# Performance work log

Hardware: AMD Instinct MI355X
Metric: run time of the kernel (lower is better)

The kernel has to match this reference:

```python
import jax, jax.numpy as jnp
import numpy as np

HID = 150

def _lstm_layer(x, Wih, Whh, bih, bhh):
    # x: [T, D] -> [T, HID]; PyTorch gate order i, f, g, o
    b = bih + bhh
    xg = x @ Wih.T + b  # precompute input contribution: [T, 4H]
    def step(carry, xg_t):
        h, c = carry
        g = xg_t + h @ Whh.T
        i, f, gg, o = jnp.split(g, 4)
        i = jax.nn.sigmoid(i); f = jax.nn.sigmoid(f)
        gg = jnp.tanh(gg); o = jax.nn.sigmoid(o)
        c = f * c + i * gg
        h = o * jnp.tanh(c)
        return (h, c), h
    init = (jnp.zeros((HID,), x.dtype), jnp.zeros((HID,), x.dtype))
    _, ys = jax.lax.scan(step, init, xg)
    return ys

def _bilstm(x, Wih, Whh, bih, bhh):
    # x: [T, D]; params stacked [L, 2, ...]
    out = x
    for l in range(Wih.shape[0]):
        fwd = _lstm_layer(out, Wih[l, 0], Whh[l, 0], bih[l, 0], bhh[l, 0])
        bwd = _lstm_layer(out[::-1], Wih[l, 1], Whh[l, 1], bih[l, 1], bhh[l, 1])[::-1]
        out = jnp.concatenate([fwd, bwd], axis=-1)  # [T, 2H]
    return out

def setup_inputs() -> dict:
    key = jax.random.key(0)
    ks = jax.random.split(key, 16)
    s = 0.1  # keep LSTM gates in a sane range
    return {
        "inputs_solv": jax.random.normal(ks[0], (1, 4096, 300), jnp.float32),
        "inputs_solu": jax.random.normal(ks[1], (1, 4096, 300), jnp.float32),
        "solv_Wih": jax.random.normal(ks[2], (2, 2, 600, 300), jnp.float32) * s,
        "solv_Whh": jax.random.normal(ks[3], (2, 2, 600, 150), jnp.float32) * s,
        "solv_bih": jax.random.normal(ks[4], (2, 2, 600), jnp.float32) * s,
        "solv_bhh": jax.random.normal(ks[5], (2, 2, 600), jnp.float32) * s,
        "solu_Wih": jax.random.normal(ks[6], (2, 2, 600, 300), jnp.float32) * s,
        "solu_Whh": jax.random.normal(ks[7], (2, 2, 600, 150), jnp.float32) * s,
        "solu_bih": jax.random.normal(ks[8], (2, 2, 600), jnp.float32) * s,
        "solu_bhh": jax.random.normal(ks[9], (2, 2, 600), jnp.float32) * s,
        "fc1_w": jax.random.normal(ks[10], (2000, 600), jnp.float32) * 0.02,
        "fc1_b": jax.random.normal(ks[11], (2000,), jnp.float32) * 0.02,
        "fc2_w": jax.random.normal(ks[12], (1, 2000), jnp.float32) * 0.02,
        "fc2_b": jax.random.normal(ks[13], (1,), jnp.float32) * 0.02,
    }

def reference(inputs_solv, inputs_solu, solv_Wih, solv_Whh, solv_bih, solv_bhh,
              solu_Wih, solu_Whh, solu_bih, solu_bhh, fc1_w, fc1_b, fc2_w, fc2_b):
    H = _bilstm(inputs_solv[0], solv_Wih, solv_Whh, solv_bih, solv_bhh)  # [Hs, 300]
    G = _bilstm(inputs_solu[0], solu_Wih, solu_Whh, solu_bih, solu_bhh)  # [Gs, 300]
    a_score = H @ G.T                      # fused version of the nested loop: [Hs, Gs]
    a = jax.nn.softmax(a_score, axis=1)
    P = a @ G                              # [Hs, 300]
    Q = a.T @ H                            # [Gs, 300]
    u = jnp.maximum(H, P)
    v = jnp.maximum(G, Q)
    inp = jnp.concatenate([u.sum(axis=0), v.sum(axis=0)], axis=0)  # [600]
    x = jax.nn.relu(inp @ fc1_w.T + fc1_b)
    return x @ fc2_w.T + fc2_b
```

## Files before the change

kernel.cpp:

```cpp
#include <hip/hip_runtime.h>
#include <hip/hip_fp16.h>
#include <cstddef>

#define T_LEN 4096
#define HID 150
#define G4 600
#define NC 300

typedef __attribute__((ext_vector_type(8))) short bf16x8;
typedef __attribute__((ext_vector_type(8))) _Float16 f16x8;
typedef __attribute__((ext_vector_type(4))) float f32x4;

__device__ __forceinline__ void barrier_lgkm() {
  asm volatile("s_waitcnt lgkmcnt(0)\n\ts_barrier" ::: "memory");
}

__device__ __forceinline__ float fsig(float x) {
  return __builtin_amdgcn_rcpf(1.f + __expf(-x));
}
__device__ __forceinline__ float ftanh(float x) {
  float ax = fabsf(x);
  float e = __expf(2.f * ax);
  float t = 1.f - 2.f * __builtin_amdgcn_rcpf(e + 1.f);
  return copysignf(t, x);
}
__device__ __forceinline__ unsigned short f2bf(float f) {
  unsigned u = __builtin_bit_cast(unsigned, f);
  u += 0x7fff + ((u >> 16) & 1);
  return (unsigned short)(u >> 16);
}

__global__ __launch_bounds__(512, 2) void lstm_scan(
    const float* __restrict__ whh_solv, const float* __restrict__ whh_solu,
    const float* __restrict__ xg_base,
    float* __restrict__ o32v, float* __restrict__ o32u,
    __half* __restrict__ o16v, __half* __restrict__ o16u, int layer, int w32)
{
  __shared__ __align__(16) unsigned short h_bf[160];
  __shared__ float g_s[640];
  const int c = blockIdx.x;
  const int net = c >> 1, dir = c & 1;
  const float* Whh = (net ? whh_solu : whh_solv) + (size_t)(layer * 2 + dir) * (G4 * HID);
  const float* xg = xg_base + (size_t)c * T_LEN * G4;
  float* out32 = (net ? o32u : o32v) + dir * HID;
  __half* out16 = (net ? o16u : o16v) + dir * HID;
  const int tid = threadIdx.x;
  const int lane = tid & 63, wv = tid >> 6;
  const int lrow = lane & 15, lq = lane >> 4;

  bf16x8 bfr[5][5];
#pragma unroll
  for (int j = 0; j < 5; j++) {
    const int jrow = 16 * (wv + 8 * j) + lrow;
#pragma unroll
    for (int kk = 0; kk < 5; kk++) {
      bf16x8 b;
#pragma unroll
      for (int i = 0; i < 8; i++) {
        const int k = kk * 32 + lq * 8 + i;
        const float v = (jrow < G4 && k < HID) ? Whh[(size_t)jrow * HID + k] : 0.f;
        b[i] = (short)f2bf(v);
      }
      bfr[j][kk] = b;
    }
  }
  if (tid < 160) h_bf[tid] = 0;
  float cst = 0.f;
  float xr0 = 0.f, xr1 = 0.f, xr2 = 0.f, xr3 = 0.f;
  if (tid < HID) {
    const int t0 = dir ? (T_LEN - 1) : 0;
    const float* xgr = xg + (size_t)t0 * G4 + tid;
    xr0 = xgr[0]; xr1 = xgr[HID]; xr2 = xgr[2 * HID]; xr3 = xgr[3 * HID];
  }
  barrier_lgkm();

  for (int s = 0; s < T_LEN; s++) {
    const int t = dir ? (T_LEN - 1 - s) : s;
    bf16x8 af[5];
#pragma unroll
    for (int kk = 0; kk < 5; kk++) {
      bf16x8 a = {0, 0, 0, 0, 0, 0, 0, 0};
      if (lrow == 0) a = *(const bf16x8*)&h_bf[kk * 32 + lq * 8];
      af[kk] = a;
    }
    f32x4 acc[5];
#pragma unroll
    for (int j = 0; j < 5; j++) acc[j] = (f32x4){0.f, 0.f, 0.f, 0.f};
#pragma unroll
    for (int kk = 0; kk < 5; kk++)
#pragma unroll
      for (int j = 0; j < 5; j++)
        acc[j] = __builtin_amdgcn_mfma_f32_16x16x32_bf16(af[kk], bfr[j][kk], acc[j], 0, 0, 0);
    if (lane < 16) {
#pragma unroll
      for (int j = 0; j < 5; j++) g_s[16 * (wv + 8 * j) + lane] = acc[j][0];
    }
    barrier_lgkm();
    if (tid < HID) {
      const int n = tid;
      float gi = xr0 + g_s[n];
      float gf = xr1 + g_s[HID + n];
      float gg = xr2 + g_s[2 * HID + n];
      float go = xr3 + g_s[3 * HID + n];
      if (s + 1 < T_LEN) {
        const int tn = dir ? (T_LEN - 2 - s) : (s + 1);
        const float* xgr = xg + (size_t)tn * G4 + n;
        xr0 = xgr[0]; xr1 = xgr[HID]; xr2 = xgr[2 * HID]; xr3 = xgr[3 * HID];
      }
      const float iv = fsig(gi), fv = fsig(gf), gv = ftanh(gg), ov = fsig(go);
      cst = fv * cst + iv * gv;
      const float hv = ov * ftanh(cst);
      h_bf[n] = f2bf(hv);
      out16[(size_t)t * 320 + n] = __float2half(hv);
      if (w32) out32[(size_t)t * NC + n] = hv;
    }
    barrier_lgkm();
  }
}

__global__ void conv_w(const float* __restrict__ wv, const float* __restrict__ wu,
                       __half* __restrict__ dst)
{
  const int gid = blockIdx.x * 256 + threadIdx.x;
  if (gid >= 8 * 640 * 320) return;
  const int k = gid % 320, j = (gid / 320) % 640, s = gid / (320 * 640);
  const int l = s >> 2, net = (s >> 1) & 1, dir = s & 1;
  float v = 0.f;
  if (j < G4 && k < NC) {
    const float* src = (net ? wu : wv) + (size_t)(l * 2 + dir) * (G4 * NC);
    v = src[(size_t)j * NC + k];
  }
  dst[gid] = __float2half(v);
}

__global__ void conv_x(const float* __restrict__ src, __half* __restrict__ dst, int rows)
{
  const int gid = blockIdx.x * 256 + threadIdx.x;
  if (gid >= rows * 320) return;
  const int k = gid % 320, m = gid / 320;
  dst[gid] = __float2half(k < NC ? src[(size_t)m * NC + k] : 0.f);
}

__global__ void conv_t(const float* __restrict__ src, __half* __restrict__ dst)
{
  const int gid = blockIdx.x * 256 + threadIdx.x;
  if (gid >= 320 * 4096) return;
  const int m = gid % 4096, f = gid / 4096;
  dst[gid] = __float2half(f < NC ? src[(size_t)m * NC + f] : 0.f);
}

__global__ void zero_f(float* __restrict__ p, int n) {
  const int i = blockIdx.x * 256 + threadIdx.x;
  if (i < n) p[i] = 0.f;
}

__global__ __launch_bounds__(256) void xg_mfma(
    const __half* __restrict__ Av, const __half* __restrict__ Au,
    const __half* __restrict__ W,
    const float* __restrict__ bihv, const float* __restrict__ bhhv,
    const float* __restrict__ bihu, const float* __restrict__ bhhu,
    float* __restrict__ xg, int layer)
{
  const int tid = threadIdx.x;
  const int lane = tid & 63, wv = tid >> 6;
  const int ln = lane & 15, q = lane >> 4;
  const int chain = blockIdx.y;
  const __half* A = (chain >= 2) ? Au : Av;
  const __half* Wc = W + (size_t)chain * 640 * 320;
  const float* bi = ((chain >= 2) ? bihu : bihv) + (size_t)(layer * 2 + (chain & 1)) * G4;
  const float* bh = ((chain >= 2) ? bhhu : bhhv) + (size_t)(layer * 2 + (chain & 1)) * G4;
  float* C = xg + (size_t)chain * T_LEN * G4;
  const int m0 = blockIdx.x * 64 + wv * 16;
  const __half* Arow = A + (size_t)(m0 + ln) * 320;

  for (int nc = 0; nc < 4; nc++) {
    f32x4 acc[10];
#pragma unroll
    for (int j = 0; j < 10; j++) acc[j] = (f32x4){0.f, 0.f, 0.f, 0.f};
    for (int kk = 0; kk < 10; kk++) {
      const f16x8 afr = *(const f16x8*)(Arow + kk * 32 + q * 8);
#pragma unroll
      for (int j = 0; j < 10; j++) {
        const int n = nc * 160 + j * 16 + ln;
        const f16x8 bfr = *(const f16x8*)(Wc + (size_t)n * 320 + kk * 32 + q * 8);
        acc[j] = __builtin_amdgcn_mfma_f32_16x16x32_f16(afr, bfr, acc[j], 0, 0, 0);
      }
    }
#pragma unroll
    for (int j = 0; j < 10; j++) {
      const int n = nc * 160 + j * 16 + ln;
      if (n < G4) {
        const float bias = bi[n] + bh[n];
#pragma unroll
        for (int r = 0; r < 4; r++)
          C[(size_t)(m0 + q * 4 + r) * G4 + n] = acc[j][r] + bias;
      }
    }
  }
}

__global__ __launch_bounds__(256) void s_gemm(
    const __half* __restrict__ Hh, const __half* __restrict__ Gh,
    __half* __restrict__ AH)
{
  const int tid = threadIdx.x;
  const int lane = tid & 63, wv = tid >> 6;
  const int ln = lane & 15, q = lane >> 4;
  const int m0 = blockIdx.x * 64 + wv * 16;
  const __half* Arow = Hh + (size_t)(m0 + ln) * 320;
  f16x8 afr[10];
#pragma unroll
  for (int kk = 0; kk < 10; kk++) afr[kk] = *(const f16x8*)(Arow + kk * 32 + q * 8);
  const int nt0 = blockIdx.y * 64;
  for (int nt = 0; nt < 64; nt++) {
    const int n = 16 * (nt0 + nt) + ln;
    const __half* Brow = Gh + (size_t)n * 320;
    f32x4 acc = (f32x4){0.f, 0.f, 0.f, 0.f};
#pragma unroll
    for (int kk = 0; kk < 10; kk++) {
      const f16x8 bfr = *(const f16x8*)(Brow + kk * 32 + q * 8);
      acc = __builtin_amdgcn_mfma_f32_16x16x32_f16(afr[kk], bfr, acc, 0, 0, 0);
    }
#pragma unroll
    for (int r = 0; r < 4; r++)
      AH[(size_t)(m0 + q * 4 + r) * 4096 + n] = __float2half(acc[r]);
  }
}

__global__ __launch_bounds__(256) void rowsum_k(const __half* __restrict__ AH,
                                                float* __restrict__ il)
{
  const int m = blockIdx.x, tid = threadIdx.x;
  const __half* row = AH + (size_t)m * 4096;
  float s = 0.f;
  for (int i = tid * 8; i < 4096; i += 2048) {
    const f16x8 v = *(const f16x8*)(row + i);
#pragma unroll
    for (int j = 0; j < 8; j++) s += __expf(fminf((float)v[j] - 30.f, 80.f));
  }
#pragma unroll
  for (int off = 32; off > 0; off >>= 1) s += __shfl_down(s, off);
  __shared__ float red[4];
  if ((tid & 63) == 0) red[tid >> 6] = s;
  __syncthreads();
  if (tid == 0) il[m] = 1.f / (red[0] + red[1] + red[2] + red[3]);
}

__global__ __launch_bounds__(256) void scale_k(__half* __restrict__ AH,
                                               const float* __restrict__ il)
{
  const size_t gid = (size_t)blockIdx.x * 256 + threadIdx.x;
  const int m = (int)(gid >> 9);
  const float ilm = il[m];
  f16x8 v = *(f16x8*)(AH + gid * 8);
#pragma unroll
  for (int j = 0; j < 8; j++)
    v[j] = (_Float16)(__expf(fminf((float)v[j] - 30.f, 80.f)) * ilm);
  *(f16x8*)(AH + gid * 8) = v;
}

__global__ __launch_bounds__(256) void pq_mfma(
    const __half* __restrict__ AH, const __half* __restrict__ GhT,
    const __half* __restrict__ HhT,
    float* __restrict__ Pb, float* __restrict__ Qb)
{
  __shared__ __align__(16) _Float16 Ats[64][72];
  const int tid = threadIdx.x;
  const int lane = tid & 63, wv = tid >> 6;
  const int ln = lane & 15, q = lane >> 4;

  if (blockIdx.x < 64) {
    const int m0 = blockIdx.x * 64 + wv * 16;
    const __half* Arow = AH + (size_t)(m0 + ln) * 4096;
    for (int nc = 0; nc < 2; nc++) {
      f32x4 acc[10];
#pragma unroll
      for (int j = 0; j < 10; j++) acc[j] = (f32x4){0.f, 0.f, 0.f, 0.f};
      for (int kk = 0; kk < 128; kk++) {
        const f16x8 afr = *(const f16x8*)(Arow + kk * 32 + q * 8);
#pragma unroll
        for (int j = 0; j < 10; j++) {
          const int n = nc * 160 + j * 16 + ln;
          const f16x8 bfr = *(const f16x8*)(GhT + (size_t)n * 4096 + kk * 32 + q * 8);
          acc[j] = __builtin_amdgcn_mfma_f32_16x16x32_f16(afr, bfr, acc[j], 0, 0, 0);
        }
      }
#pragma unroll
      for (int j = 0; j < 10; j++) {
        const int n = nc * 160 + j * 16 + ln;
        if (n < NC) {
#pragma unroll
          for (int r = 0; r < 4; r++)
            Pb[(size_t)(m0 + q * 4 + r) * NC + n] = acc[j][r];
        }
      }
    }
  } else {
    const int j0 = (blockIdx.x - 64) * 64;
    f32x4 acc[20];
#pragma unroll
    for (int j = 0; j < 20; j++) acc[j] = (f32x4){0.f, 0.f, 0.f, 0.f};
    const int il8 = tid >> 2, j8 = (tid & 3) * 16;
    for (int ic = 0; ic < 4096; ic += 64) {
      __syncthreads();
      {
        const __half* src = AH + (size_t)(ic + il8) * 4096 + j0 + j8;
        const f16x8 v0 = *(const f16x8*)src;
        const f16x8 v1 = *(const f16x8*)(src + 8);
#pragma unroll
        for (int jj = 0; jj < 8; jj++) Ats[j8 + jj][il8] = v0[jj];
#pragma unroll
        for (int jj = 0; jj < 8; jj++) Ats[j8 + 8 + jj][il8] = v1[jj];
      }
      __syncthreads();
#pragma unroll
      for (int s = 0; s < 2; s++) {
        const f16x8 afr = *(const f16x8*)&Ats[wv * 16 + ln][s * 32 + q * 8];
        const __half* bbase = HhT + ic + s * 32 + q * 8;
#pragma unroll
        for (int j = 0; j < 20; j++) {
          const f16x8 bfr = *(const f16x8*)(bbase + (size_t)(j * 16 + ln) * 4096);
          acc[j] = __builtin_amdgcn_mfma_f32_16x16x32_f16(afr, bfr, acc[j], 0, 0, 0);
        }
      }
    }
#pragma unroll
    for (int j = 0; j < 20; j++) {
      const int f = j * 16 + ln;
      if (f < NC) {
#pragma unroll
        for (int r = 0; r < 4; r++)
          Qb[(size_t)(j0 + wv * 16 + q * 4 + r) * NC + f] = acc[j][r];
      }
    }
  }
}

__global__ void reduce_uv(const float* __restrict__ X, const float* __restrict__ Yp,
                          float* __restrict__ inp, int off)
{
  const int j = threadIdx.x;
  if (j >= NC) return;
  const int r0 = blockIdx.x * 128;
  float s = 0.f;
  for (int r = r0; r < r0 + 128; r++)
    s += fmaxf(X[(size_t)r * NC + j], Yp[(size_t)r * NC + j]);
  atomicAdd(&inp[off + j], s);
}

__global__ void fc1_k(const float* __restrict__ w1, const float* __restrict__ b1,
                      const float* __restrict__ inp, float* __restrict__ x)
{
  const int r = blockIdx.x * 256 + threadIdx.x;
  if (r >= 2000) return;
  float s = b1[r];
  const float* wr = w1 + (size_t)r * 600;
  for (int k = 0; k < 600; k++) s += wr[k] * inp[k];
  x[r] = fmaxf(s, 0.f);
}

__global__ void fc2_k(const float* __restrict__ x, const float* __restrict__ w2,
                      const float* __restrict__ b2, float* __restrict__ outp)
{
  const int tid = threadIdx.x;
  float s = 0.f;
  for (int i = tid; i < 2000; i += 256) s += x[i] * w2[i];
#pragma unroll
  for (int off = 32; off > 0; off >>= 1) s += __shfl_down(s, off);
  __shared__ float red[4];
  if ((tid & 63) == 0) red[tid >> 6] = s;
  __syncthreads();
  if (tid == 0) outp[0] = red[0] + red[1] + red[2] + red[3] + b2[0];
}

extern "C" void kernel_launch(void* const* d_in, const int* in_sizes, int n_in,
                              void* d_out, int out_size, void* d_ws, size_t ws_size,
                              hipStream_t stream)
{
  const float* in_solv  = (const float*)d_in[0];
  const float* in_solu  = (const float*)d_in[1];
  const float* solv_Wih = (const float*)d_in[2];
  const float* solv_Whh = (const float*)d_in[3];
  const float* solv_bih = (const float*)d_in[4];
  const float* solv_bhh = (const float*)d_in[5];
  const float* solu_Wih = (const float*)d_in[6];
  const float* solu_Whh = (const float*)d_in[7];
  const float* solu_bih = (const float*)d_in[8];
  const float* solu_bhh = (const float*)d_in[9];
  const float* fc1_w = (const float*)d_in[10];
  const float* fc1_b = (const float*)d_in[11];
  const float* fc2_w = (const float*)d_in[12];
  const float* fc2_b = (const float*)d_in[13];
  float* outp = (float*)d_out;
  float* ws = (float*)d_ws;

  constexpr size_t off_P   = 0;
  constexpr size_t off_Q   = 1228800;
  constexpr size_t off_inp = 2457600;
  constexpr size_t off_x   = 2458240;
  constexpr size_t off_il  = 2460288;
  constexpr size_t off_xg  = 2468480;
  constexpr size_t off_L0  = off_xg + (size_t)4 * 2457600;
  constexpr size_t off_HG  = off_L0 + 1310720;

  float*  xg   = ws + off_xg;
  float*  Hb   = ws + off_HG;
  float*  Gb   = Hb + 1228800;
  float*  Pb   = ws + off_P;
  float*  Qb   = ws + off_Q;
  float*  inp  = ws + off_inp;
  float*  xf   = ws + off_x;
  float*  il   = ws + off_il;
  __half* Wihh = (__half*)(ws + off_P);
  __half* Avh  = (__half*)(ws + off_L0);
  __half* Auh  = Avh + 4096 * 320;
  __half* L0vh = (__half*)(ws + off_HG);
  __half* L0uh = L0vh + 4096 * 320;
  __half* Hh   = (__half*)(ws + off_L0);
  __half* Gh   = Hh + 4096 * 320;
  __half* AH   = (__half*)(ws + off_xg);
  __half* HhT  = AH + (size_t)4096 * 4096;
  __half* GhT  = HhT + 320 * 4096;

  zero_f<<<5120, 256, 0, stream>>>(ws + off_HG, 1310720);
  conv_w<<<(8 * 640 * 320 + 255) / 256, 256, 0, stream>>>(solv_Wih, solu_Wih, Wihh);
  conv_x<<<5120, 256, 0, stream>>>(in_solv, Avh, 4096);
  conv_x<<<5120, 256, 0, stream>>>(in_solu, Auh, 4096);

  xg_mfma<<<dim3(64, 4), 256, 0, stream>>>(Avh, Auh, Wihh,
      solv_bih, solv_bhh, solu_bih, solu_bhh, xg, 0);
  lstm_scan<<<4, 512, 0, stream>>>(solv_Whh, solu_Whh, xg,
      nullptr, nullptr, L0vh, L0uh, 0, 0);

  xg_mfma<<<dim3(64, 4), 256, 0, stream>>>(L0vh, L0uh, Wihh + (size_t)4 * 640 * 320,
      solv_bih, solv_bhh, solu_bih, solu_bhh, xg, 1);
  lstm_scan<<<4, 512, 0, stream>>>(solv_Whh, solu_Whh, xg,
      Hb, Gb, Hh, Gh, 1, 1);

  conv_t<<<5120, 256, 0, stream>>>(Hb, HhT);
  conv_t<<<5120, 256, 0, stream>>>(Gb, GhT);
  s_gemm<<<dim3(64, 4), 256, 0, stream>>>(Hh, Gh, AH);
  rowsum_k<<<4096, 256, 0, stream>>>(AH, il);
  scale_k<<<8192, 256, 0, stream>>>(AH, il);
  pq_mfma<<<128, 256, 0, stream>>>(AH, GhT, HhT, Pb, Qb);

  zero_f<<<3, 256, 0, stream>>>(inp, 640);
  reduce_uv<<<32, 320, 0, stream>>>(Hb, Pb, inp, 0);
  reduce_uv<<<32, 320, 0, stream>>>(Gb, Qb, inp, 300);
  fc1_k<<<8, 256, 0, stream>>>(fc1_w, fc1_b, inp, xf);
  fc2_k<<<1, 256, 0, stream>>>(xf, fc2_w, fc2_b, outp);
}
```

Before: 7.062 ms.

## Swap MFMA operands so gate quadruples land in registers and drop one barrier

```diff
diff --git a/kernel.cpp b/kernel.cpp
--- a/kernel.cpp
+++ b/kernel.cpp
@@ -36,8 +36,7 @@
     float* __restrict__ o32v, float* __restrict__ o32u,
     __half* __restrict__ o16v, __half* __restrict__ o16u, int layer, int w32)
 {
-  __shared__ __align__(16) unsigned short h_bf[160];
-  __shared__ float g_s[640];
+  __shared__ __align__(16) unsigned short hbuf[2][160];
   const int c = blockIdx.x;
   const int net = c >> 1, dir = c & 1;
   const float* Whh = (net ? whh_solu : whh_solv) + (size_t)(layer * 2 + dir) * (G4 * HID);
@@ -48,41 +47,44 @@
   const int lane = tid & 63, wv = tid >> 6;
   const int lrow = lane & 15, lq = lane >> 4;
 
-  bf16x8 bfr[5][5];
+  bf16x8 wfr[5][5];
 #pragma unroll
   for (int j = 0; j < 5; j++) {
-    const int jrow = 16 * (wv + 8 * j) + lrow;
+    const int T = wv + 8 * j;
+    const int un = 4 * T + (lrow >> 2);
+    const int gt = lrow & 3;
 #pragma unroll
     for (int kk = 0; kk < 5; kk++) {
       bf16x8 b;
 #pragma unroll
       for (int i = 0; i < 8; i++) {
         const int k = kk * 32 + lq * 8 + i;
-        const float v = (jrow < G4 && k < HID) ? Whh[(size_t)jrow * HID + k] : 0.f;
+        const float v = (un < HID && k < HID) ? Whh[(size_t)(gt * HID + un) * HID + k] : 0.f;
         b[i] = (short)f2bf(v);
       }
-      bfr[j][kk] = b;
-    }
-  }
-  if (tid < 160) h_bf[tid] = 0;
+      wfr[j][kk] = b;
+    }
+  }
+  if (tid < 160) hbuf[0][tid] = 0;
+
+  const int u = 4 * (wv + 8 * lrow) + lq;
   float cst = 0.f;
   float xr0 = 0.f, xr1 = 0.f, xr2 = 0.f, xr3 = 0.f;
-  if (tid < HID) {
+  if (lrow < 5 && u < HID) {
     const int t0 = dir ? (T_LEN - 1) : 0;
-    const float* xgr = xg + (size_t)t0 * G4 + tid;
+    const float* xgr = xg + (size_t)t0 * G4 + u;
     xr0 = xgr[0]; xr1 = xgr[HID]; xr2 = xgr[2 * HID]; xr3 = xgr[3 * HID];
   }
   barrier_lgkm();
 
   for (int s = 0; s < T_LEN; s++) {
     const int t = dir ? (T_LEN - 1 - s) : s;
-    bf16x8 af[5];
-#pragma unroll
-    for (int kk = 0; kk < 5; kk++) {
-      bf16x8 a = {0, 0, 0, 0, 0, 0, 0, 0};
-      if (lrow == 0) a = *(const bf16x8*)&h_bf[kk * 32 + lq * 8];
-      af[kk] = a;
-    }
+    const unsigned short* hc = hbuf[s & 1];
+    unsigned short* hn = hbuf[(s & 1) ^ 1];
+    bf16x8 hb[5];
+#pragma unroll
+    for (int kk = 0; kk < 5; kk++)
+      hb[kk] = *(const bf16x8*)&hc[kk * 32 + lq * 8];
     f32x4 acc[5];
 #pragma unroll
     for (int j = 0; j < 5; j++) acc[j] = (f32x4){0.f, 0.f, 0.f, 0.f};
@@ -90,29 +92,28 @@
     for (int kk = 0; kk < 5; kk++)
 #pragma unroll
       for (int j = 0; j < 5; j++)
-        acc[j] = __builtin_amdgcn_mfma_f32_16x16x32_bf16(af[kk], bfr[j][kk], acc[j], 0, 0, 0);
-    if (lane < 16) {
-#pragma unroll
-      for (int j = 0; j < 5; j++) g_s[16 * (wv + 8 * j) + lane] = acc[j][0];
-    }
-    barrier_lgkm();
-    if (tid < HID) {
-      const int n = tid;
-      float gi = xr0 + g_s[n];
-      float gf = xr1 + g_s[HID + n];
-      float gg = xr2 + g_s[2 * HID + n];
-      float go = xr3 + g_s[3 * HID + n];
-      if (s + 1 < T_LEN) {
+        acc[j] = __builtin_amdgcn_mfma_f32_16x16x32_bf16(wfr[j][kk], hb[kk], acc[j], 0, 0, 0);
+    if (lrow < 5) {
+      float gi = 0.f, gf = 0.f, gg = 0.f, go = 0.f;
+#pragma unroll
+      for (int j = 0; j < 5; j++)
+        if (lrow == j) { gi = acc[j][0]; gf = acc[j][1]; gg = acc[j][2]; go = acc[j][3]; }
+      gi += xr0; gf += xr1; gg += xr2; go += xr3;
+      if (s + 1 < T_LEN && u < HID) {
         const int tn = dir ? (T_LEN - 2 - s) : (s + 1);
-        const float* xgr = xg + (size_t)tn * G4 + n;
+        const float* xgr = xg + (size_t)tn * G4 + u;
         xr0 = xgr[0]; xr1 = xgr[HID]; xr2 = xgr[2 * HID]; xr3 = xgr[3 * HID];
       }
       const float iv = fsig(gi), fv = fsig(gf), gv = ftanh(gg), ov = fsig(go);
       cst = fv * cst + iv * gv;
       const float hv = ov * ftanh(cst);
-      h_bf[n] = f2bf(hv);
-      out16[(size_t)t * 320 + n] = __float2half(hv);
-      if (w32) out32[(size_t)t * NC + n] = hv;
+      unsigned short hw = 0;
+      if (u < HID) {
+        hw = f2bf(hv);
+        out16[(size_t)t * 320 + u] = __float2half(hv);
+        if (w32) out32[(size_t)t * NC + u] = hv;
+      }
+      hn[u] = hw;
     }
     barrier_lgkm();
   }
```

New measurement: 8.876 ms. +25.7%, slower.
